# Optimization experiments

Hardware: AMD Instinct MI355X
Metric: run time of the kernel (lower is better)

Reference implementation:

```python
import jax, jax.numpy as jnp
import numpy as np

MIN_WEIGHT = 0.0
MAX_WEIGHT = 500.0


def setup_inputs() -> dict:
    key = jax.random.key(0)
    k1, k2, k3 = jax.random.split(key, 3)
    B, P = 131072, 64   # groundings, predicates
    C, L = 128, 3       # clauses, literals per clause
    ground_atoms = jax.random.normal(k1, (B, P), dtype=jnp.float32)
    # learned clause weights, initial_clause_weight = 0.5
    clause_weights = 0.5 * jnp.ones((C,), dtype=jnp.float32)
    # which predicate each literal refers to
    literal_idx = jax.random.randint(k2, (C, L), 0, P, dtype=jnp.int64)
    # 0 -> negated literal (sign -1), 1 -> positive literal (sign +1)
    sign_bits = jax.random.randint(k3, (C, L), 0, 2, dtype=jnp.int32)
    return {
        "ground_atoms": ground_atoms,
        "clause_weights": clause_weights,
        "literal_idx": literal_idx,
        "sign_bits": sign_bits,
    }


def reference(ground_atoms, clause_weights, literal_idx, sign_bits):
    """Vectorized KnowledgeEnhancer forward.

    Per clause (GodelBoostConormApprox):
      literals = signs * ground_atoms[:, idx]
      delta    = signs * clamp(w) * softmax(literals)
    Then concat all clause deltas and scatter_add into predicate space.
    """
    B, P = ground_atoms.shape
    C, L = literal_idx.shape
    signs = (2 * sign_bits - 1).astype(ground_atoms.dtype)  # [C, L] in {-1,+1}
    gathered = ground_atoms[:, literal_idx]                 # [B, C, L] gather
    literals = signs[None, :, :] * gathered                 # signed pre-activations
    w = jnp.clip(clause_weights, MIN_WEIGHT, MAX_WEIGHT)    # [C]
    delta = signs[None, :, :] * w[None, :, None] * jax.nn.softmax(literals, axis=-1)
    # concat over clauses (dim=1 in the torch code) then scatter_add over predicates
    delta_flat = delta.reshape(B, C * L)
    idx_flat = literal_idx.reshape(C * L)
    out = jax.ops.segment_sum(delta_flat.T, idx_flat, num_segments=P)  # [P, B]
    return out.T  # [B, P]
```

## Files before the change

### kernel.cpp

```cpp
#include <hip/hip_runtime.h>
#include <stdint.h>

typedef unsigned int  u32;
typedef unsigned short u16;

#define B_ROWS 131072
#define P_PRED 64
#define C_CLS  128
#define NPAIR  384
#define CAP    32
#define RPB    128
#define TPB    512
#define GCAP   104
#define LOG2E  1.4426950408889634f

#if __has_builtin(__builtin_amdgcn_exp2f)
#define EXP2F(x) __builtin_amdgcn_exp2f(x)
#else
#define EXP2F(x) exp2f(x)
#endif

#if __has_builtin(__builtin_amdgcn_rcpf)
#define RCPF(x) __builtin_amdgcn_rcpf(x)
#else
#define RCPF(x) (1.0f / (x))
#endif

__device__ __forceinline__ float bf16_to_f(u16 u) {
    return __uint_as_float(((u32)u) << 16);
}
__device__ __forceinline__ u16 f_to_bf16(float f) {
    u32 u = __float_as_uint(f);
    u += 0x7FFFu + ((u >> 16) & 1u);
    return (u16)(u >> 16);
}

__global__ void ke_prep(const u32* __restrict__ lidx_w,
                        const u32* __restrict__ sb_w,
                        const u32* __restrict__ w_w,
                        uint2* __restrict__ stream,
                        u32* __restrict__ cnt8w,
                        u32* __restrict__ flags) {
    __shared__ int scnt[P_PRED];
    __shared__ u32 recPk[P_PRED][CAP];
    __shared__ float recW[P_PRED][CAP];
    __shared__ int sidx[NPAIR];
    __shared__ int ssb[NPAIR];
    __shared__ int det[3];
    const int t = threadIdx.x;
    if (t < P_PRED) scnt[t] = 0;
    if (t < 3) det[t] = 1;
    __syncthreads();
    if (t < NPAIR / 2) {
        if (lidx_w[2 * t + 1] != 0u) det[0] = 0;
        if (sb_w[2 * t + 1]   != 0u) det[1] = 0;
    }
    if (t == 0 && (w_w[0] & 0xFFFFu) == 0u) det[2] = 0;
    __syncthreads();
    if (t < NPAIR) {
        sidx[t] = (int)(det[0] ? lidx_w[2 * t] : lidx_w[t]);
        ssb[t]  = (int)(det[1] ? sb_w[2 * t]   : sb_w[t]);
    }
    __syncthreads();
    if (t < NPAIR) {
        const int c = t / 3;
        const int l = t - c * 3;
        const int base = c * 3;
        const int o1 = base + (l == 0 ? 1 : 0);
        const int o2 = base + (l == 2 ? 1 : 2);
        const int p = sidx[t];
        const int slot = atomicAdd(&scnt[p], 1);
        float wraw = det[2] ? bf16_to_f((u16)(w_w[c / 2] >> ((c & 1) * 16)))
                            : __uint_as_float(w_w[c]);
        float wc = fminf(fmaxf(wraw, 0.0f), 500.0f);
        if (slot < CAP) {
            u32 s1 = 2u * (u32)sidx[o1] + (ssb[o1] ? 0u : 1u);
            u32 s2 = 2u * (u32)sidx[o2] + (ssb[o2] ? 0u : 1u);
            recPk[p][slot] = (ssb[t] ? 0u : 1u) | (s1 << 8) | (s2 << 16);
            recW[p][slot]  = ssb[t] ? wc : -wc;
        }
    }
    __syncthreads();
    if (t < P_PRED) {
        const int p = t;
        const int g = p >> 3;
        const int n = min(scnt[p], CAP);
        int off = 0;
        for (int pb = g * 8; pb < p; ++pb) off += min(scnt[pb], CAP);
        int ncl = 0;
        for (int j = 0; j < n; ++j) {
            if (off + j < GCAP) {
                stream[g * GCAP + off + j] =
                    make_uint2(recPk[p][j], __float_as_uint(recW[p][j]));
                ++ncl;
            }
        }
        ((unsigned char*)cnt8w)[p] = (unsigned char)ncl;
    }
    if (t == 0) flags[0] = (u32)det[2];
}

__global__ __launch_bounds__(TPB, 8)
void ke_main(const void* __restrict__ atoms_v,
             const uint2* __restrict__ stream_g,
             const u32* __restrict__ cnt8w,
             const u32* __restrict__ flags,
             void* __restrict__ out_v) {
    __shared__ u16 E2[2 * P_PRED * RPB];
    __shared__ uint2 srec[8 * GCAP];
    __shared__ unsigned char cnt8[P_PRED];
    const int tid = threadIdx.x;
    const int lane = tid & 63;
    const int g = __builtin_amdgcn_readfirstlane(tid >> 6);
    const int rowBase = blockIdx.x * RPB;
    const bool bf16m = (flags[0] != 0u);

    for (int i = tid; i < 8 * GCAP; i += TPB) srec[i] = stream_g[i];
    if (tid < 16) ((u32*)cnt8)[tid] = cnt8w[tid];

    {
        const int r = tid & 127;
        const int c0 = (tid >> 7) * 16;
        if (bf16m) {
            const u16* gp = (const u16*)atoms_v + (size_t)(rowBase + r) * P_PRED + c0;
            uint4 v0 = *(const uint4*)gp;
            uint4 v1 = *(const uint4*)(gp + 8);
            u32 w[8] = {v0.x, v0.y, v0.z, v0.w, v1.x, v1.y, v1.z, v1.w};
#pragma unroll
            for (int k = 0; k < 8; ++k) {
                float xlo = __uint_as_float(w[k] << 16) * LOG2E;
                float xhi = __uint_as_float(w[k] & 0xFFFF0000u) * LOG2E;
                float elo = EXP2F(xlo), ehi = EXP2F(xhi);
                const int sl = 2 * (c0 + 2 * k);
                E2[(sl)     * RPB + r] = f_to_bf16(elo);
                E2[(sl + 1) * RPB + r] = f_to_bf16(RCPF(elo));
                E2[(sl + 2) * RPB + r] = f_to_bf16(ehi);
                E2[(sl + 3) * RPB + r] = f_to_bf16(RCPF(ehi));
            }
        } else {
            const float* gp = (const float*)atoms_v + (size_t)(rowBase + r) * P_PRED + c0;
#pragma unroll
            for (int k4 = 0; k4 < 4; ++k4) {
                float4 v = *(const float4*)(gp + 4 * k4);
                float xs[4] = {v.x, v.y, v.z, v.w};
#pragma unroll
                for (int k = 0; k < 4; ++k) {
                    float e = EXP2F(xs[k] * LOG2E);
                    const int sl = 2 * (c0 + 4 * k4 + k);
                    E2[(sl)     * RPB + r] = f_to_bf16(e);
                    E2[(sl + 1) * RPB + r] = f_to_bf16(RCPF(e));
                }
            }
        }
    }
    __syncthreads();

    const int q2 = 2 * lane;
    float2 acc[8];
    int j = g * GCAP;

#pragma unroll
    for (int pp = 0; pp < 8; ++pp) {
        const int p = g * 8 + pp;
        const u32 eppv = *(const u32*)&E2[(2 * p)     * RPB + q2];
        const u32 epnv = *(const u32*)&E2[(2 * p + 1) * RPB + q2];
        const float eppx = __uint_as_float(eppv << 16);
        const float eppy = __uint_as_float(eppv & 0xFFFF0000u);
        const float epnx = __uint_as_float(epnv << 16);
        const float epny = __uint_as_float(epnv & 0xFFFF0000u);
        const int n = (int)cnt8[p];
        float2 a = make_float2(0.0f, 0.0f);

#define REC_BODY(J)                                                           \
        {                                                                     \
            const uint2 rec = srec[J];                  \
            const u32 pk = rec.x;                                             \
            const float sw = __uint_as_float(rec.y);                          \
            const u32 s1v = *(const u32*)&E2[(int)((pk >> 8)  & 255u) * RPB + q2]; \
            const u32 s2v = *(const u32*)&E2[(int)((pk >> 16) & 255u) * RPB + q2]; \
            const float ssx = (pk & 1u) ? epnx : eppx;                        \
            const float ssy = (pk & 1u) ? epny : eppy;                        \
            const float s1x = __uint_as_float(s1v << 16);                     \
            const float s1y = __uint_as_float(s1v & 0xFFFF0000u);             \
            const float s2x = __uint_as_float(s2v << 16);                     \
            const float s2y = __uint_as_float(s2v & 0xFFFF0000u);             \
            const float tx = RCPF(ssx + s1x + s2x);                           \
            const float ty = RCPF(ssy + s1y + s2y);                          \
            a.x = fmaf(sw * ssx, tx, a.x);                                    \
            a.y = fmaf(sw * ssy, ty, a.y);                                    \
        }

        int e = 0;
        for (; e + 1 < n; e += 2) {
            REC_BODY(j)
            REC_BODY(j + 1)
            j += 2;
        }
        if (e < n) { REC_BODY(j) ++j; }
#undef REC_BODY
        acc[pp] = a;
    }

    if (bf16m) {
        u16* op0 = (u16*)out_v + (size_t)(rowBase + q2) * P_PRED + g * 8;
        u16* op1 = op0 + P_PRED;
        uint4 o0, o1v;
        o0.x  = (u32)f_to_bf16(acc[0].x) | ((u32)f_to_bf16(acc[1].x) << 16);
        o0.y  = (u32)f_to_bf16(acc[2].x) | ((u32)f_to_bf16(acc[3].x) << 16);
        o0.z  = (u32)f_to_bf16(acc[4].x) | ((u32)f_to_bf16(acc[5].x) << 16);
        o0.w  = (u32)f_to_bf16(acc[6].x) | ((u32)f_to_bf16(acc[7].x) << 16);
        o1v.x = (u32)f_to_bf16(acc[0].y) | ((u32)f_to_bf16(acc[1].y) << 16);
        o1v.y = (u32)f_to_bf16(acc[2].y) | ((u32)f_to_bf16(acc[3].y) << 16);
        o1v.z = (u32)f_to_bf16(acc[4].y) | ((u32)f_to_bf16(acc[5].y) << 16);
        o1v.w = (u32)f_to_bf16(acc[6].y) | ((u32)f_to_bf16(acc[7].y) << 16);
        *(uint4*)op0 = o0;
        *(uint4*)op1 = o1v;
    } else {
        float* op0 = (float*)out_v + (size_t)(rowBase + q2) * P_PRED + g * 8;
        float* op1 = op0 + P_PRED;
        *(float4*)(op0)     = make_float4(acc[0].x, acc[1].x, acc[2].x, acc[3].x);
        *(float4*)(op0 + 4) = make_float4(acc[4].x, acc[5].x, acc[6].x, acc[7].x);
        *(float4*)(op1)     = make_float4(acc[0].y, acc[1].y, acc[2].y, acc[3].y);
        *(float4*)(op1 + 4) = make_float4(acc[4].y, acc[5].y, acc[6].y, acc[7].y);
    }
}

extern "C" void kernel_launch(void* const* d_in, const int* in_sizes, int n_in,
                              void* d_out, int out_size, void* d_ws, size_t ws_size,
                              hipStream_t stream_h) {
    const u32* clause_weights = (const u32*)d_in[1];
    const u32* literal_idx    = (const u32*)d_in[2];
    const u32* sign_bits      = (const u32*)d_in[3];

    uint2* stream = (uint2*)d_ws;
    u32*   cnt8w  = (u32*)((char*)d_ws + 8 * GCAP * 8);
    u32*   flags  = (u32*)((char*)d_ws + 8 * GCAP * 8 + 64);

    ke_prep<<<1, NPAIR, 0, stream_h>>>(literal_idx, sign_bits, clause_weights,
                                       stream, cnt8w, flags);
    ke_main<<<B_ROWS / RPB, TPB, 0, stream_h>>>(d_in[0], stream, cnt8w, flags,
                                                d_out);
}
```

Before: 103.0 us.

## Repack exp tables as row-pair words, split accumulators, stage bf16 output via LDS

```diff
diff --git a/kernel.cpp b/kernel.cpp
--- a/kernel.cpp
+++ b/kernel.cpp
@@ -12,6 +12,7 @@
 #define RPB    128
 #define TPB    512
 #define GCAP   104
+#define OSTR   33
 #define LOG2E  1.4426950408889634f
 
 #if __has_builtin(__builtin_amdgcn_exp2f)
@@ -33,6 +34,9 @@
     u32 u = __float_as_uint(f);
     u += 0x7FFFu + ((u >> 16) & 1u);
     return (u16)(u >> 16);
+}
+__device__ __forceinline__ u32 pack_bf16x2(float lo, float hi) {
+    return (u32)f_to_bf16(lo) | ((u32)f_to_bf16(hi) << 16);
 }
 
 __global__ void ke_prep(const u32* __restrict__ lidx_w,
@@ -106,9 +110,10 @@
              const u32* __restrict__ cnt8w,
              const u32* __restrict__ flags,
              void* __restrict__ out_v) {
-    __shared__ u16 E2[2 * P_PRED * RPB];
+    __shared__ u32 smem32[8192];
     __shared__ uint2 srec[8 * GCAP];
     __shared__ unsigned char cnt8[P_PRED];
+    u16* E2 = (u16*)smem32;
     const int tid = threadIdx.x;
     const int lane = tid & 63;
     const int g = __builtin_amdgcn_readfirstlane(tid >> 6);
@@ -119,37 +124,43 @@
     if (tid < 16) ((u32*)cnt8)[tid] = cnt8w[tid];
 
     {
-        const int r = tid & 127;
-        const int c0 = (tid >> 7) * 16;
+        const int a = tid & 63;
+        const int c0 = (tid >> 6) * 8;
         if (bf16m) {
-            const u16* gp = (const u16*)atoms_v + (size_t)(rowBase + r) * P_PRED + c0;
-            uint4 v0 = *(const uint4*)gp;
-            uint4 v1 = *(const uint4*)(gp + 8);
-            u32 w[8] = {v0.x, v0.y, v0.z, v0.w, v1.x, v1.y, v1.z, v1.w};
-#pragma unroll
-            for (int k = 0; k < 8; ++k) {
-                float xlo = __uint_as_float(w[k] << 16) * LOG2E;
-                float xhi = __uint_as_float(w[k] & 0xFFFF0000u) * LOG2E;
-                float elo = EXP2F(xlo), ehi = EXP2F(xhi);
-                const int sl = 2 * (c0 + 2 * k);
-                E2[(sl)     * RPB + r] = f_to_bf16(elo);
-                E2[(sl + 1) * RPB + r] = f_to_bf16(RCPF(elo));
-                E2[(sl + 2) * RPB + r] = f_to_bf16(ehi);
-                E2[(sl + 3) * RPB + r] = f_to_bf16(RCPF(ehi));
+            const u16* gp0 = (const u16*)atoms_v + (size_t)(rowBase + 2 * a) * P_PRED + c0;
+            uint4 v0 = *(const uint4*)gp0;
+            uint4 v1 = *(const uint4*)(gp0 + P_PRED);
+            u32 w0[4] = {v0.x, v0.y, v0.z, v0.w};
+            u32 w1[4] = {v1.x, v1.y, v1.z, v1.w};
+#pragma unroll
+            for (int k = 0; k < 4; ++k) {
+                float xl0 = __uint_as_float(w0[k] << 16) * LOG2E;
+                float xh0 = __uint_as_float(w0[k] & 0xFFFF0000u) * LOG2E;
+                float xl1 = __uint_as_float(w1[k] << 16) * LOG2E;
+                float xh1 = __uint_as_float(w1[k] & 0xFFFF0000u) * LOG2E;
+                float el0 = EXP2F(xl0), eh0 = EXP2F(xh0);
+                float el1 = EXP2F(xl1), eh1 = EXP2F(xh1);
+                const int m = c0 + 2 * k;
+                smem32[(2 * m)     * 64 + a] = pack_bf16x2(el0, el1);
+                smem32[(2 * m + 1) * 64 + a] = pack_bf16x2(RCPF(el0), RCPF(el1));
+                smem32[(2 * m + 2) * 64 + a] = pack_bf16x2(eh0, eh1);
+                smem32[(2 * m + 3) * 64 + a] = pack_bf16x2(RCPF(eh0), RCPF(eh1));
             }
         } else {
-            const float* gp = (const float*)atoms_v + (size_t)(rowBase + r) * P_PRED + c0;
-#pragma unroll
-            for (int k4 = 0; k4 < 4; ++k4) {
-                float4 v = *(const float4*)(gp + 4 * k4);
-                float xs[4] = {v.x, v.y, v.z, v.w};
-#pragma unroll
-                for (int k = 0; k < 4; ++k) {
-                    float e = EXP2F(xs[k] * LOG2E);
-                    const int sl = 2 * (c0 + 4 * k4 + k);
-                    E2[(sl)     * RPB + r] = f_to_bf16(e);
-                    E2[(sl + 1) * RPB + r] = f_to_bf16(RCPF(e));
-                }
+            const float* gp0 = (const float*)atoms_v + (size_t)(rowBase + 2 * a) * P_PRED + c0;
+            float4 u0 = *(const float4*)gp0;
+            float4 u1 = *(const float4*)(gp0 + 4);
+            float4 d0 = *(const float4*)(gp0 + P_PRED);
+            float4 d1 = *(const float4*)(gp0 + P_PRED + 4);
+            float r0[8] = {u0.x, u0.y, u0.z, u0.w, u1.x, u1.y, u1.z, u1.w};
+            float r1[8] = {d0.x, d0.y, d0.z, d0.w, d1.x, d1.y, d1.z, d1.w};
+#pragma unroll
+            for (int k = 0; k < 8; ++k) {
+                float e0 = EXP2F(r0[k] * LOG2E);
+                float e1 = EXP2F(r1[k] * LOG2E);
+                const int m = c0 + k;
+                smem32[(2 * m)     * 64 + a] = pack_bf16x2(e0, e1);
+                smem32[(2 * m + 1) * 64 + a] = pack_bf16x2(RCPF(e0), RCPF(e1));
             }
         }
     }
@@ -169,11 +180,12 @@
         const float epnx = __uint_as_float(epnv << 16);
         const float epny = __uint_as_float(epnv & 0xFFFF0000u);
         const int n = (int)cnt8[p];
-        float2 a = make_float2(0.0f, 0.0f);
-
-#define REC_BODY(J)                                                           \
+        float2 a0 = make_float2(0.0f, 0.0f);
+        float2 a1 = make_float2(0.0f, 0.0f);
+
+#define REC_BODY(J, A)                                                        \
         {                                                                     \
-            const uint2 rec = srec[J];                  \
+            const uint2 rec = srec[J];                     \
             const u32 pk = rec.x;                                             \
             const float sw = __uint_as_float(rec.y);                          \
             const u32 s1v = *(const u32*)&E2[(int)((pk >> 8)  & 255u) * RPB + q2]; \
@@ -186,35 +198,42 @@
             const float s2y = __uint_as_float(s2v & 0xFFFF0000u);             \
             const float tx = RCPF(ssx + s1x + s2x);                           \
             const float ty = RCPF(ssy + s1y + s2y);                          \
-            a.x = fmaf(sw * ssx, tx, a.x);                                    \
-            a.y = fmaf(sw * ssy, ty, a.y);                                    \
+            A.x = fmaf(sw * ssx, tx, A.x);                                    \
+            A.y = fmaf(sw * ssy, ty, A.y);                                    \
         }
 
         int e = 0;
-        for (; e + 1 < n; e += 2) {
-            REC_BODY(j)
-            REC_BODY(j + 1)
-            j += 2;
-        }
-        if (e < n) { REC_BODY(j) ++j; }
+        for (; e + 3 < n; e += 4) {
+            REC_BODY(j,     a0)
+            REC_BODY(j + 1, a1)
+            REC_BODY(j + 2, a0)
+            REC_BODY(j + 3, a1)
+            j += 4;
+        }
+        for (; e < n; ++e, ++j) REC_BODY(j, a0)
 #undef REC_BODY
-        acc[pp] = a;
+        acc[pp] = make_float2(a0.x + a1.x, a0.y + a1.y);
     }
 
     if (bf16m) {
-        u16* op0 = (u16*)out_v + (size_t)(rowBase + q2) * P_PRED + g * 8;
-        u16* op1 = op0 + P_PRED;
-        uint4 o0, o1v;
-        o0.x  = (u32)f_to_bf16(acc[0].x) | ((u32)f_to_bf16(acc[1].x) << 16);
-        o0.y  = (u32)f_to_bf16(acc[2].x) | ((u32)f_to_bf16(acc[3].x) << 16);
-        o0.z  = (u32)f_to_bf16(acc[4].x) | ((u32)f_to_bf16(acc[5].x) << 16);
-        o0.w  = (u32)f_to_bf16(acc[6].x) | ((u32)f_to_bf16(acc[7].x) << 16);
-        o1v.x = (u32)f_to_bf16(acc[0].y) | ((u32)f_to_bf16(acc[1].y) << 16);
-        o1v.y = (u32)f_to_bf16(acc[2].y) | ((u32)f_to_bf16(acc[3].y) << 16);
-        o1v.z = (u32)f_to_bf16(acc[4].y) | ((u32)f_to_bf16(acc[5].y) << 16);
-        o1v.w = (u32)f_to_bf16(acc[6].y) | ((u32)f_to_bf16(acc[7].y) << 16);
-        *(uint4*)op0 = o0;
-        *(uint4*)op1 = o1v;
+        __syncthreads();
+        u32* OutT = smem32;
+#pragma unroll
+        for (int k = 0; k < 4; ++k) {
+            u32 lo = pack_bf16x2(acc[2 * k].x, acc[2 * k + 1].x);
+            u32 hi = pack_bf16x2(acc[2 * k].y, acc[2 * k + 1].y);
+            OutT[(q2)     * OSTR + g * 4 + k] = lo;
+            OutT[(q2 + 1) * OSTR + g * 4 + k] = hi;
+        }
+        __syncthreads();
+        const int erow = tid >> 2;
+        const int qt = tid & 3;
+        const u32* src = &OutT[erow * OSTR + qt * 8];
+        uint4 o0 = make_uint4(src[0], src[1], src[2], src[3]);
+        uint4 o1 = make_uint4(src[4], src[5], src[6], src[7]);
+        u16* op = (u16*)out_v + (size_t)(rowBase + erow) * P_PRED + qt * 16;
+        *(uint4*)op       = o0;
+        *(uint4*)(op + 8) = o1;
     } else {
         float* op0 = (float*)out_v + (size_t)(rowBase + q2) * P_PRED + g * 8;
         float* op1 = op0 + P_PRED;
```

After: 105.4 us. 2.3% more time.
